# Performance work log

Hardware: AMD Instinct MI355X
Metric: run time of the kernel (lower is better)

Reference implementation:

```python
import jax, jax.numpy as jnp
import numpy as np

B, T, D = 8, 1024, 512
H = 8
F_OUT = D // H          # 64 per head
ALPHA = 0.2             # LeakyReLU slope in GAT
MASK_RATE = 0.3
GAMMA = 0.0625          # DistanceAdj gamma
BIAS = 0.2              # DistanceAdj bias
LN_EPS = 1e-5
NEG_INF = -9e15
L2_EPS = 1e-12          # F.normalize eps


def setup_inputs() -> dict:
    key = jax.random.key(0)
    ks = jax.random.split(key, 8)
    return {
        "x": jax.random.normal(ks[0], (B, T, D), jnp.float32),
        "W": jax.random.normal(ks[1], (H, D, F_OUT), jnp.float32) * 0.05,
        "a_src": jax.random.normal(ks[2], (H, F_OUT), jnp.float32) * 0.05,
        "a_dst": jax.random.normal(ks[3], (H, F_OUT), jnp.float32) * 0.05,
        "W2": jax.random.normal(ks[4], (D, D), jnp.float32) * 0.02,
        "b2": jnp.zeros((D,), jnp.float32),
        "ln_g": jnp.ones((D,), jnp.float32),
        "ln_b": jnp.zeros((D,), jnp.float32),
    }


def _distance_adj(batch, t):
    # DistanceAdj: Gaussian kernel over temporal index distance, shared across batch
    idx = jnp.arange(t, dtype=jnp.float32)
    d2 = (idx[:, None] - idx[None, :]) ** 2
    adj = jnp.exp(-GAMMA * d2 - BIAS)                      # [T, T]
    return jnp.broadcast_to(adj[None], (batch, t, t))      # [B, T, T]


def reference(x, W, a_src, a_dst, W2, b2, ln_g, ln_b):
    b, t, d = x.shape
    adj = _distance_adj(b, t)

    # top-k magnitude node selection -> row/col union mask (index_fill loop)
    k = int(MASK_RATE * t)
    mags = jnp.linalg.norm(x, axis=2)                      # [B, T]
    _, topk = jax.lax.top_k(mags, k)                       # [B, k]
    sel = jnp.zeros((b, t), bool).at[jnp.arange(b)[:, None], topk].set(True)
    mask = sel[:, :, None] | sel[:, None, :]               # rows OR cols filled
    adj = jnp.where(mask, adj, 0.0)

    # GAT multi-head attention (dense masked form, dropout=0 at eval)
    Wh = jnp.einsum("btd,hdf->bhtf", x, W)                 # [B,H,T,F']
    e_src = jnp.einsum("bhtf,hf->bht", Wh, a_src)
    e_dst = jnp.einsum("bhtf,hf->bht", Wh, a_dst)
    e = jax.nn.leaky_relu(e_src[..., :, None] + e_dst[..., None, :], ALPHA)
    e = jnp.where(adj[:, None] > 0, e, NEG_INF)            # masked logits
    attn = jax.nn.softmax(e, axis=-1)                      # [B,H,T,T]
    hp = jnp.einsum("bhts,bhsf->bhtf", attn, Wh)
    hp = jax.nn.elu(hp)                                    # concat=True -> elu per head
    tmp = hp.transpose(0, 2, 1, 3).reshape(b, t, d)        # concat heads -> [B,T,512]

    # signed-sqrt + F.normalize (default dim=1 -> over T axis)
    tmp = jnp.sqrt(jax.nn.relu(tmp)) - jnp.sqrt(jax.nn.relu(-tmp))
    nrm = jnp.linalg.norm(tmp, axis=1, keepdims=True)      # [B,1,D]
    tmp = tmp / jnp.maximum(nrm, L2_EPS)

    # residual linear + LayerNorm + permute
    y = x + tmp @ W2 + b2
    mu = jnp.mean(y, axis=-1, keepdims=True)
    var = jnp.mean((y - mu) ** 2, axis=-1, keepdims=True)
    y = (y - mu) / jnp.sqrt(var + LN_EPS) * ln_g + ln_b
    return y.transpose(0, 2, 1)                            # [B, D, T]
```

## Files before the change

kernel.cpp:

```cpp
#include <hip/hip_runtime.h>
#include <hip/hip_bf16.h>

typedef unsigned short u16;
typedef short bf16x8 __attribute__((ext_vector_type(8)));
typedef float f32x4 __attribute__((ext_vector_type(4)));
typedef int   i32x4 __attribute__((ext_vector_type(4)));

#define NB 8
#define NT 1024
#define ND 512
#define KSEL 307
#define PSTR 152
#define TSTR 136

__device__ __forceinline__ float bf2f(u16 u){
  union { unsigned int i; float f; } c; c.i = ((unsigned int)u) << 16; return c.f;
}
__device__ __forceinline__ u16 f2bf(float f){
  __hip_bfloat16 h = __float2bfloat16(f);
  u16 u; __builtin_memcpy(&u, &h, 2); return u;
}

__global__ void k_select(const float* __restrict__ mags, int* __restrict__ sel){
  __shared__ float sm[NT];
  int b = blockIdx.x;
  int tid = threadIdx.x;
  for (int i = tid; i < NT; i += 256) sm[i] = mags[b * NT + i];
  __syncthreads();
  int tl = tid >> 2, tq = tid & 3;
  int t = blockIdx.y * 64 + tl;
  float m = sm[t];
  int cnt = 0;
  int s0 = tq * 256;
  for (int s = s0; s < s0 + 256; s++){
    float v = sm[s];
    cnt += (v > m) || (v == m && s < t);
  }
  cnt += __shfl_xor(cnt, 1, 64);
  cnt += __shfl_xor(cnt, 2, 64);
  if (tq == 0) sel[b * NT + t] = (cnt < KSEL) ? 1 : 0;
}

__launch_bounds__(256, 3)
__global__ void k_gemm_wh(const float* __restrict__ x, const float* __restrict__ Wf,
                          const float* __restrict__ W2f,
                          const float* __restrict__ a_src, const float* __restrict__ a_dst,
                          u16* __restrict__ WhT, float* __restrict__ es, float* __restrict__ ed,
                          float* __restrict__ mags, float* __restrict__ cn,
                          u16* __restrict__ W2T){
  __shared__ u16 smem[8704];
  u16* As = smem;
  u16* Bs = smem + 5120;
  int m0 = blockIdx.x * 128;
  int h  = blockIdx.y;
  int tid = threadIdx.x;
  if (h == 0 && tid < 64) cn[blockIdx.x * 64 + tid] = 0.f;
  if (h == 2){
    float* tile = (float*)smem;
    int kt0 = (blockIdx.x >> 3) * 64, n00 = (blockIdx.x & 7) * 64;
    int r = tid >> 6, cl = tid & 63;
#pragma unroll
    for (int p = 0; p < 16; p++)
      tile[(r + p*4)*65 + cl] = W2f[(size_t)(kt0 + r + p*4) * 512 + n00 + cl];
    __syncthreads();
#pragma unroll
    for (int p = 0; p < 16; p++){
      int orow = r + p*4;
      W2T[(size_t)(n00 + orow) * 512 + kt0 + cl] = f2bf(tile[cl*65 + orow]);
    }
    __syncthreads();
  }
  int wv = tid >> 6, lane = tid & 63;
  int quad = lane >> 4, lr = lane & 15;
  f32x4 acc[2][4] = {};
  float sq[2] = {0.f, 0.f};
  int ar = (tid * 8) >> 5, ac = (tid * 8) & 31;
  const float* xa0 = &x[(size_t)(m0 + ar) * 512 + ac];
  const float* xa1 = xa0 + (size_t)64 * 512;
  int kk = (tid * 8) >> 6, f0 = (tid * 8) & 63;
  const float* wb = &Wf[((size_t)h << 15) + (size_t)kk * 64 + f0];
  int bbase = f0 * 40 + (((kk >> 3) ^ ((f0 >> 3) & 3)) * 8) + (kk & 7);
  f32x4 pa0 = *(const f32x4*)xa0, pa1 = *(const f32x4*)(xa0 + 4);
  f32x4 pa2 = *(const f32x4*)xa1, pa3 = *(const f32x4*)(xa1 + 4);
  f32x4 pb0 = *(const f32x4*)wb,  pb1 = *(const f32x4*)(wb + 4);
  for (int kt = 0; kt < 512; kt += 32){
    __syncthreads();
    {
      u16 pk[8];
      if (h == 0){
#pragma unroll
        for (int q = 0; q < 4; q++) sq[0] += pa0[q]*pa0[q] + pa1[q]*pa1[q];
#pragma unroll
        for (int q = 0; q < 4; q++) sq[1] += pa2[q]*pa2[q] + pa3[q]*pa3[q];
      }
#pragma unroll
      for (int q = 0; q < 4; q++){ pk[q] = f2bf(pa0[q]); pk[4+q] = f2bf(pa1[q]); }
      *(bf16x8*)&As[ar*40 + ac] = *(const bf16x8*)pk;
#pragma unroll
      for (int q = 0; q < 4; q++){ pk[q] = f2bf(pa2[q]); pk[4+q] = f2bf(pa3[q]); }
      *(bf16x8*)&As[(ar + 64)*40 + ac] = *(const bf16x8*)pk;
#pragma unroll
      for (int q = 0; q < 4; q++) Bs[bbase + q*40]       = f2bf(pb0[q]);
#pragma unroll
      for (int q = 0; q < 4; q++) Bs[bbase + (q+4)*40]   = f2bf(pb1[q]);
    }
    __syncthreads();
    if (kt < 480){
      pa0 = *(const f32x4*)(xa0 + kt + 32); pa1 = *(const f32x4*)(xa0 + kt + 36);
      pa2 = *(const f32x4*)(xa1 + kt + 32); pa3 = *(const f32x4*)(xa1 + kt + 36);
      pb0 = *(const f32x4*)(wb + (size_t)(kt + 32) * 64);
      pb1 = *(const f32x4*)(wb + (size_t)(kt + 32) * 64 + 4);
    }
    bf16x8 af[2], bfr[4];
#pragma unroll
    for (int i = 0; i < 2; i++) af[i] = *(const bf16x8*)&As[(wv*32 + i*16 + lr)*40 + quad*8];
#pragma unroll
    for (int i = 0; i < 4; i++){
      int f = i*16 + lr;
      bfr[i] = *(const bf16x8*)&Bs[f*40 + ((quad ^ ((f >> 3) & 3)) * 8)];
    }
#pragma unroll
    for (int mi = 0; mi < 2; mi++)
#pragma unroll
      for (int ni = 0; ni < 4; ni++)
        acc[mi][ni] = __builtin_amdgcn_mfma_f32_16x16x32_bf16(af[mi], bfr[ni], acc[mi][ni], 0, 0, 0);
  }
  if (h == 0){
#pragma unroll
    for (int i = 0; i < 2; i++){
      float s = sq[i];
      s += __shfl_xor(s, 1, 64);
      s += __shfl_xor(s, 2, 64);
      if ((tid & 3) == 0) mags[m0 + i*64 + (tid >> 2)] = sqrtf(s);
    }
  }
  float asv[4], adv[4];
#pragma unroll
  for (int ni = 0; ni < 4; ni++){
    asv[ni] = a_src[h*64 + ni*16 + lr];
    adv[ni] = a_dst[h*64 + ni*16 + lr];
  }
#pragma unroll
  for (int mi = 0; mi < 2; mi++)
#pragma unroll
    for (int r = 0; r < 4; r++){
      float pes = 0.f, ped = 0.f;
#pragma unroll
      for (int ni = 0; ni < 4; ni++){
        pes += acc[mi][ni][r] * asv[ni];
        ped += acc[mi][ni][r] * adv[ni];
      }
#pragma unroll
      for (int mofs = 1; mofs < 16; mofs <<= 1){
        pes += __shfl_xor(pes, mofs, 64);
        ped += __shfl_xor(ped, mofs, 64);
      }
      if (lr == 0){
        int rowg = m0 + wv*32 + mi*16 + quad*4 + r;
        int bb_ = rowg >> 10, tt = rowg & 1023;
        es[(bb_ * 8 + h) * NT + tt] = pes;
        ed[(bb_ * 8 + h) * NT + tt] = ped;
      }
    }
  __syncthreads();
  u16* Tr = smem;
#pragma unroll
  for (int mi = 0; mi < 2; mi++)
#pragma unroll
    for (int ni = 0; ni < 4; ni++){
      int fl = ni*16 + lr;
      int tl = wv*32 + mi*16 + quad*4;
#pragma unroll
      for (int r = 0; r < 4; r++) Tr[fl*TSTR + tl + r] = f2bf(acc[mi][ni][r]);
    }
  __syncthreads();
  int f = tid >> 2, seg = tid & 3;
  int b_ = m0 >> 10;
  u16* dst = &WhT[(b_ * 512 + h * 64 + f) * NT + (m0 & 1023) + seg*32];
  const u16* srcp = &Tr[f*TSTR + seg*32];
#pragma unroll
  for (int k8 = 0; k8 < 4; k8++)
    *(bf16x8*)(dst + k8*8) = *(const bf16x8*)(srcp + k8*8);
}

__launch_bounds__(256)
__global__ void k_attn(const u16* __restrict__ WhT, const float* __restrict__ es,
                       const float* __restrict__ ed, const int* __restrict__ sel,
                       u16* __restrict__ t2b, float* __restrict__ cn){
  __shared__ u16 P[64 * PSTR];
  __shared__ float edw[144];
  __shared__ int   selw[144];
  __shared__ float esw[64];
  __shared__ float swv[64];
  int bh = blockIdx.x;
  int b = bh >> 3;
  int t0 = blockIdx.y * 64;
  int tid = threadIdx.x;
  int wv = tid >> 6, lane = tid & 63;
  int quad = lane >> 4, lr = lane & 15;
  int s_base = t0 - 40;
  for (int i = tid; i < 144; i += 256){
    int s = s_base + i;
    bool ok = (s >= 0 && s < NT);
    edw[i]  = ok ? ed[bh * NT + s] : 0.f;
    selw[i] = ok ? sel[b * NT + s] : 0;
  }
  if (tid < 64) esw[tid] = es[bh * NT + t0 + tid];
  {
    i32x4 z = {};
    for (int i = lane; i < 304; i += 64){
      int r16 = i / 19, c16 = i - r16 * 19;
      *(i32x4*)&P[(16*wv + r16) * PSTR + c16 * 8] = z;
    }
  }
  __syncthreads();
  {
    int tl = 16*wv + (lane >> 2);
    int q = lane & 3;
    float e_t = esw[tl];
    int sel_t = selw[tl + 40];
    float part = 0.f;
    for (int j = q; j <= 80; j += 4){
      int sw = tl + j;
      int s = s_base + sw;
      float w = 0.f;
      if (s >= 0 && s < NT && (sel_t | selw[sw])){
        float v = e_t + edw[sw];
        v = v > 0.f ? v : 0.2f * v;
        v = fminf(v, 60.f);
        w = bf2f(f2bf(__expf(v)));
      }
      part += w;
      if (w != 0.f) P[tl * PSTR + sw] = f2bf(w);
    }
    part += __shfl_xor(part, 1, 64);
    part += __shfl_xor(part, 2, 64);
    if (q == 0) swv[tl] = part;
  }
  __syncthreads();
  f32x4 acc[4] = {};
  const u16* vbase = WhT + (bh * 64) * NT;
#pragma unroll
  for (int ks = 0; ks < 96; ks += 32){
    bf16x8 afr = *(const bf16x8*)&P[(16*wv + lr) * PSTR + 16*wv + ks + quad*8];
    int tb = s_base + 16*wv + ks + quad*8;
    bool ok = (tb >= 0) && (tb < NT);
    bf16x8 zf = {};
#pragma unroll
    for (int jn = 0; jn < 4; jn++){
      bf16x8 bfr = ok ? *(const bf16x8*)&vbase[(16*jn + lr) * NT + tb] : zf;
      acc[jn] = __builtin_amdgcn_mfma_f32_16x16x32_bf16(afr, bfr, acc[jn], 0, 0, 0);
    }
  }
#pragma unroll
  for (int jn = 0; jn < 4; jn++){
    float ssum = 0.f;
#pragma unroll
    for (int r = 0; r < 4; r++){
      int t_loc = 16*wv + quad*4 + r;
      float sw_ = swv[t_loc];
      float hp = acc[jn][r] / (sw_ > 0.f ? sw_ : 1.f);
      hp = hp > 0.f ? hp : (__expf(hp) - 1.f);
      float o = hp >= 0.f ? sqrtf(hp) : -sqrtf(-hp);
      ssum += o * o;
      t2b[(b * NT + t0 + t_loc) * ND + (bh & 7) * 64 + 16*jn + lr] = f2bf(o);
    }
    ssum += __shfl_xor(ssum, 16, 64);
    ssum += __shfl_xor(ssum, 32, 64);
    if (quad == 0) atomicAdd(&cn[b * ND + (bh & 7) * 64 + 16*jn + lr], ssum);
  }
}

__launch_bounds__(512)
__global__ void k_gemm2ln(const u16* __restrict__ A, const u16* __restrict__ W2T,
                          const float* __restrict__ xres, const float* __restrict__ b2,
                          const float* __restrict__ cn, const float* __restrict__ g,
                          const float* __restrict__ bb, float* __restrict__ out){
  __shared__ __align__(16) char smraw[69888];
  u16*   As  = (u16*)smraw;
  u16*   Bs  = (u16*)(smraw + 2560);
  float* scl = (float*)(smraw + 43520);
  float* T     = (float*)smraw;
  float* wpart = (float*)(smraw + 67584);
  float* mus   = (float*)(smraw + 69632);
  float* rss   = (float*)(smraw + 69760);
  int tid = threadIdx.x;
  int m0 = blockIdx.x * 32;
  int b  = m0 >> 10, t0 = m0 & 1023;
  int w = tid >> 6, lane = tid & 63;
  int quad = lane >> 4, lr = lane & 15;
  {
    float nv = sqrtf(cn[(b << 9) + tid]);
    scl[tid] = 1.f / fmaxf(nv, 1e-12f);
  }
  int ar = tid >> 2, ac = (tid & 3) * 8;
  const u16* ap = &A[(size_t)(m0 + ar) * 512 + ac];
  int nb_ = tid >> 2, c = (tid & 3) * 8;
  bf16x8 ra = {}, rb[4];
  if (tid < 128) ra = __builtin_nontemporal_load((const bf16x8*)ap);
#pragma unroll
  for (int rep = 0; rep < 4; rep++)
    rb[rep] = *(const bf16x8*)&W2T[(size_t)(nb_ + rep*128) * 512 + c];
  f32x4 acc[2][4] = {};
  for (int kt = 0; kt < 512; kt += 32){
    __syncthreads();
    if (tid < 128){
      u16 pk[8];
#pragma unroll
      for (int q = 0; q < 8; q++)
        pk[q] = f2bf(bf2f((u16)ra[q]) * scl[kt + ac + q]);
      *(bf16x8*)&As[ar*40 + ac] = *(const bf16x8*)pk;
    }
#pragma unroll
    for (int rep = 0; rep < 4; rep++)
      *(bf16x8*)&Bs[(nb_ + rep*128)*40 + c] = rb[rep];
    __syncthreads();
    if (kt < 480){
      if (tid < 128) ra = __builtin_nontemporal_load((const bf16x8*)(ap + kt + 32));
#pragma unroll
      for (int rep = 0; rep < 4; rep++)
        rb[rep] = *(const bf16x8*)&W2T[(size_t)(nb_ + rep*128) * 512 + kt + 32 + c];
    }
    bf16x8 af[2], bfr[4];
#pragma unroll
    for (int mi = 0; mi < 2; mi++) af[mi] = *(const bf16x8*)&As[(mi*16 + lr)*40 + quad*8];
#pragma unroll
    for (int i = 0; i < 4; i++)
      bfr[i] = *(const bf16x8*)&Bs[(w*64 + i*16 + lr)*40 + quad*8];
#pragma unroll
    for (int mi = 0; mi < 2; mi++)
#pragma unroll
      for (int ni = 0; ni < 4; ni++)
        acc[mi][ni] = __builtin_amdgcn_mfma_f32_16x16x32_bf16(af[mi], bfr[ni], acc[mi][ni], 0, 0, 0);
  }
  float b2v[4];
#pragma unroll
  for (int ni = 0; ni < 4; ni++) b2v[ni] = b2[w*64 + ni*16 + lr];
  float yv[2][4][4];
#pragma unroll
  for (int mi = 0; mi < 2; mi++)
#pragma unroll
    for (int r = 0; r < 4; r++){
      int rl = mi*16 + quad*4 + r;
      float rs = 0.f, rq = 0.f;
#pragma unroll
      for (int ni = 0; ni < 4; ni++){
        int col = w*64 + ni*16 + lr;
        float v = acc[mi][ni][r]
                + __builtin_nontemporal_load(&xres[(size_t)(m0 + rl) * 512 + col])
                + b2v[ni];
        yv[mi][ni][r] = v;
        rs += v; rq += v * v;
      }
#pragma unroll
      for (int m2 = 1; m2 < 16; m2 <<= 1){
        rs += __shfl_xor(rs, m2, 64);
        rq += __shfl_xor(rq, m2, 64);
      }
      if (lr == 0){
        wpart[w*32 + rl]       = rs;
        wpart[256 + w*32 + rl] = rq;
      }
    }
  __syncthreads();
  if (tid < 32){
    float s = 0.f, q = 0.f;
#pragma unroll
    for (int wv2 = 0; wv2 < 8; wv2++){
      s += wpart[wv2*32 + tid];
      q += wpart[256 + wv2*32 + tid];
    }
    float mu = s * (1.f/512.f);
    float var = q * (1.f/512.f) - mu * mu;
    mus[tid] = mu;
    rss[tid] = 1.f / sqrtf(var + 1e-5f);
  }
  __syncthreads();
  float gv[4], bv[4];
#pragma unroll
  for (int ni = 0; ni < 4; ni++){
    gv[ni] = g[w*64 + ni*16 + lr];
    bv[ni] = bb[w*64 + ni*16 + lr];
  }
#pragma unroll
  for (int mi = 0; mi < 2; mi++)
#pragma unroll
    for (int r = 0; r < 4; r++){
      int rl = mi*16 + quad*4 + r;
      float mu = mus[rl], rstd = rss[rl];
#pragma unroll
      for (int ni = 0; ni < 4; ni++){
        int col = w*64 + ni*16 + lr;
        T[col*33 + rl] = (yv[mi][ni][r] - mu) * rstd * gv[ni] + bv[ni];
      }
    }
  __syncthreads();
  int j = tid & 31, dq = tid >> 5;
#pragma unroll
  for (int kk2 = 0; kk2 < 32; kk2++){
    int d = dq + kk2 * 16;
    __builtin_nontemporal_store(T[d*33 + j],
        &out[((size_t)(b * 512 + d)) * 1024 + t0 + j]);
  }
}

extern "C" void kernel_launch(void* const* d_in, const int* in_sizes, int n_in,
                              void* d_out, int out_size, void* d_ws, size_t ws_size,
                              hipStream_t stream) {
  (void)in_sizes; (void)n_in; (void)out_size; (void)ws_size;
  const float* x     = (const float*)d_in[0];
  const float* W     = (const float*)d_in[1];
  const float* a_src = (const float*)d_in[2];
  const float* a_dst = (const float*)d_in[3];
  const float* W2    = (const float*)d_in[4];
  const float* b2    = (const float*)d_in[5];
  const float* ln_g  = (const float*)d_in[6];
  const float* ln_b  = (const float*)d_in[7];
  char* ws = (char*)d_ws;
  int*   sel   = (int*)  (ws + 256);
  float* mags  = (float*)(ws + 33024);
  float* es    = (float*)(ws + 1124608);
  float* ed    = (float*)(ws + 1386752);
  float* cn    = (float*)(ws + 1648896);
  u16*   WhT   = (u16*)  (ws + 2097152);
  u16*   t2b   = (u16*)  (ws + 18874368);
  u16*   W2T   = (u16*)  (ws + 36175872);
  float* out   = (float*)d_out;

  k_gemm_wh  <<<dim3(64, 8), 256, 0, stream>>>(x, W, W2, a_src, a_dst, WhT, es, ed, mags, cn, W2T);
  k_select   <<<dim3(NB, 16), 256, 0, stream>>>(mags, sel);
  k_attn     <<<dim3(64, 16), 256, 0, stream>>>(WhT, es, ed, sel, t2b, cn);
  k_gemm2ln  <<<dim3(256), 512, 0, stream>>>(t2b, W2T, x, b2, cn, ln_g, ln_b, out);
}
```

Baseline: 144.0 us.

## Split K of output GEMM across two thread groups in 1024-thread blocks

The W2 projection+LayerNorm kernel now launches 1024 threads per block, and two 512-thread groups each handle half of the K dimension with separate LDS tiles. The second group writes its partial accumulators to shared memory, where the first group sums them before the residual, LayerNorm and transposed store. The aim is to halve the serial K loop per block and raise wave count with only 256 blocks in the grid. In exchange it uses more shared memory per block, adds an LDS reduction and extra barriers, and leaves half the threads idle during the epilogue.

Result: no change. 144.0 us (+0.0%).

```diff
diff --git a/kernel.cpp b/kernel.cpp
--- a/kernel.cpp
+++ b/kernel.cpp
@@ -271,55 +271,63 @@
   }
 }
 
-__launch_bounds__(512)
+__launch_bounds__(1024, 4)
 __global__ void k_gemm2ln(const u16* __restrict__ A, const u16* __restrict__ W2T,
                           const float* __restrict__ xres, const float* __restrict__ b2,
                           const float* __restrict__ cn, const float* __restrict__ g,
                           const float* __restrict__ bb, float* __restrict__ out){
-  __shared__ __align__(16) char smraw[69888];
-  u16*   As  = (u16*)smraw;
-  u16*   Bs  = (u16*)(smraw + 2560);
-  float* scl = (float*)(smraw + 43520);
-  float* T     = (float*)smraw;
-  float* wpart = (float*)(smraw + 67584);
-  float* mus   = (float*)(smraw + 69632);
-  float* rss   = (float*)(smraw + 69760);
+  __shared__ __align__(16) char smraw[91392];
+  u16* As0 = (u16*)smraw;
+  u16* As1 = (u16*)(smraw + 2560);
+  u16* Bs0 = (u16*)(smraw + 5120);
+  u16* Bs1 = (u16*)(smraw + 46080);
+  float* scl   = (float*)(smraw + 87040);
+  float* wpart = (float*)(smraw + 89088);
+  float* mus   = (float*)(smraw + 91136);
+  float* rss   = (float*)(smraw + 91264);
+  float* accbuf = (float*)(smraw + 5120);
+  float* T      = (float*)smraw;
   int tid = threadIdx.x;
+  int gid = tid >> 9;
+  int l   = tid & 511;
   int m0 = blockIdx.x * 32;
   int b  = m0 >> 10, t0 = m0 & 1023;
-  int w = tid >> 6, lane = tid & 63;
-  int quad = lane >> 4, lr = lane & 15;
-  {
+  int w = l >> 6;
+  int lane = tid & 63, quad = lane >> 4, lr = lane & 15;
+  u16* As = gid ? As1 : As0;
+  u16* Bs = gid ? Bs1 : Bs0;
+  int kb = gid << 8;
+  if (tid < 512){
     float nv = sqrtf(cn[(b << 9) + tid]);
     scl[tid] = 1.f / fmaxf(nv, 1e-12f);
   }
-  int ar = tid >> 2, ac = (tid & 3) * 8;
-  const u16* ap = &A[(size_t)(m0 + ar) * 512 + ac];
-  int nb_ = tid >> 2, c = (tid & 3) * 8;
+  int ar = l >> 2, ac = (l & 3) * 8;
+  const u16* ap = &A[(size_t)(m0 + ar) * 512 + kb + ac];
+  int nb_ = l >> 2, c = (l & 3) * 8;
   bf16x8 ra = {}, rb[4];
-  if (tid < 128) ra = __builtin_nontemporal_load((const bf16x8*)ap);
+  if (l < 128) ra = *(const bf16x8*)ap;
 #pragma unroll
   for (int rep = 0; rep < 4; rep++)
-    rb[rep] = *(const bf16x8*)&W2T[(size_t)(nb_ + rep*128) * 512 + c];
+    rb[rep] = *(const bf16x8*)&W2T[(size_t)(nb_ + rep*128) * 512 + kb + c];
   f32x4 acc[2][4] = {};
-  for (int kt = 0; kt < 512; kt += 32){
-    __syncthreads();
-    if (tid < 128){
+  for (int kt = 0; kt < 256; kt += 32){
+    __syncthreads();
+    if (l < 128){
       u16 pk[8];
 #pragma unroll
       for (int q = 0; q < 8; q++)
-        pk[q] = f2bf(bf2f((u16)ra[q]) * scl[kt + ac + q]);
+        pk[q] = f2bf(bf2f((u16)ra[q]) * scl[kb + kt + ac + q]);
       *(bf16x8*)&As[ar*40 + ac] = *(const bf16x8*)pk;
     }
 #pragma unroll
     for (int rep = 0; rep < 4; rep++)
       *(bf16x8*)&Bs[(nb_ + rep*128)*40 + c] = rb[rep];
     __syncthreads();
-    if (kt < 480){
-      if (tid < 128) ra = __builtin_nontemporal_load((const bf16x8*)(ap + kt + 32));
+    if (kt < 224){
+      if (l < 128) ra = *(const bf16x8*)(ap + kt + 32);
 #pragma unroll
       for (int rep = 0; rep < 4; rep++)
-        rb[rep] = *(const bf16x8*)&W2T[(size_t)(nb_ + rep*128) * 512 + kt + 32 + c];
+        rb[rep] = *(const bf16x8*)&W2T[(size_t)(nb_ + rep*128) * 512 + kb + kt + 32 + c];
     }
     bf16x8 af[2], bfr[4];
 #pragma unroll
@@ -333,35 +341,49 @@
       for (int ni = 0; ni < 4; ni++)
         acc[mi][ni] = __builtin_amdgcn_mfma_f32_16x16x32_bf16(af[mi], bfr[ni], acc[mi][ni], 0, 0, 0);
   }
-  float b2v[4];
-#pragma unroll
-  for (int ni = 0; ni < 4; ni++) b2v[ni] = b2[w*64 + ni*16 + lr];
+  __syncthreads();
+  if (gid == 1){
+    float* dst = &accbuf[l * 33];
+#pragma unroll
+    for (int mi = 0; mi < 2; mi++)
+#pragma unroll
+      for (int ni = 0; ni < 4; ni++)
+#pragma unroll
+        for (int r = 0; r < 4; r++)
+          dst[mi*16 + ni*4 + r] = acc[mi][ni][r];
+  }
+  __syncthreads();
   float yv[2][4][4];
-#pragma unroll
-  for (int mi = 0; mi < 2; mi++)
-#pragma unroll
-    for (int r = 0; r < 4; r++){
-      int rl = mi*16 + quad*4 + r;
-      float rs = 0.f, rq = 0.f;
-#pragma unroll
-      for (int ni = 0; ni < 4; ni++){
-        int col = w*64 + ni*16 + lr;
-        float v = acc[mi][ni][r]
-                + __builtin_nontemporal_load(&xres[(size_t)(m0 + rl) * 512 + col])
-                + b2v[ni];
-        yv[mi][ni][r] = v;
-        rs += v; rq += v * v;
-      }
-#pragma unroll
-      for (int m2 = 1; m2 < 16; m2 <<= 1){
-        rs += __shfl_xor(rs, m2, 64);
-        rq += __shfl_xor(rq, m2, 64);
-      }
-      if (lr == 0){
-        wpart[w*32 + rl]       = rs;
-        wpart[256 + w*32 + rl] = rq;
-      }
-    }
+  if (gid == 0){
+    const float* src = &accbuf[l * 33];
+    float b2v[4];
+#pragma unroll
+    for (int ni = 0; ni < 4; ni++) b2v[ni] = b2[w*64 + ni*16 + lr];
+#pragma unroll
+    for (int mi = 0; mi < 2; mi++)
+#pragma unroll
+      for (int r = 0; r < 4; r++){
+        int rl = mi*16 + quad*4 + r;
+        float rs = 0.f, rq = 0.f;
+#pragma unroll
+        for (int ni = 0; ni < 4; ni++){
+          int col = w*64 + ni*16 + lr;
+          float v = acc[mi][ni][r] + src[mi*16 + ni*4 + r]
+                  + xres[(size_t)(m0 + rl) * 512 + col] + b2v[ni];
+          yv[mi][ni][r] = v;
+          rs += v; rq += v * v;
+        }
+#pragma unroll
+        for (int m2 = 1; m2 < 16; m2 <<= 1){
+          rs += __shfl_xor(rs, m2, 64);
+          rq += __shfl_xor(rq, m2, 64);
+        }
+        if (lr == 0){
+          wpart[w*32 + rl]       = rs;
+          wpart[256 + w*32 + rl] = rq;
+        }
+      }
+  }
   __syncthreads();
   if (tid < 32){
     float s = 0.f, q = 0.f;
@@ -376,29 +398,31 @@
     rss[tid] = 1.f / sqrtf(var + 1e-5f);
   }
   __syncthreads();
-  float gv[4], bv[4];
-#pragma unroll
-  for (int ni = 0; ni < 4; ni++){
-    gv[ni] = g[w*64 + ni*16 + lr];
-    bv[ni] = bb[w*64 + ni*16 + lr];
-  }
-#pragma unroll
-  for (int mi = 0; mi < 2; mi++)
-#pragma unroll
-    for (int r = 0; r < 4; r++){
-      int rl = mi*16 + quad*4 + r;
-      float mu = mus[rl], rstd = rss[rl];
-#pragma unroll
-      for (int ni = 0; ni < 4; ni++){
-        int col = w*64 + ni*16 + lr;
-        T[col*33 + rl] = (yv[mi][ni][r] - mu) * rstd * gv[ni] + bv[ni];
-      }
-    }
+  if (gid == 0){
+    float gv[4], bv[4];
+#pragma unroll
+    for (int ni = 0; ni < 4; ni++){
+      gv[ni] = g[w*64 + ni*16 + lr];
+      bv[ni] = bb[w*64 + ni*16 + lr];
+    }
+#pragma unroll
+    for (int mi = 0; mi < 2; mi++)
+#pragma unroll
+      for (int r = 0; r < 4; r++){
+        int rl = mi*16 + quad*4 + r;
+        float mu = mus[rl], rstd = rss[rl];
+#pragma unroll
+        for (int ni = 0; ni < 4; ni++){
+          int col = w*64 + ni*16 + lr;
+          T[col*33 + rl] = (yv[mi][ni][r] - mu) * rstd * gv[ni] + bv[ni];
+        }
+      }
+  }
   __syncthreads();
   int j = tid & 31, dq = tid >> 5;
 #pragma unroll
-  for (int kk2 = 0; kk2 < 32; kk2++){
-    int d = dq + kk2 * 16;
+  for (int kk2 = 0; kk2 < 16; kk2++){
+    int d = dq + kk2 * 32;
     __builtin_nontemporal_store(T[d*33 + j],
         &out[((size_t)(b * 512 + d)) * 1024 + t0 + j]);
   }
@@ -430,5 +454,5 @@
   k_gemm_wh  <<<dim3(64, 8), 256, 0, stream>>>(x, W, W2, a_src, a_dst, WhT, es, ed, mags, cn, W2T);
   k_select   <<<dim3(NB, 16), 256, 0, stream>>>(mags, sel);
   k_attn     <<<dim3(64, 16), 256, 0, stream>>>(WhT, es, ed, sel, t2b, cn);
-  k_gemm2ln  <<<dim3(256), 512, 0, stream>>>(t2b, W2T, x, b2, cn, ln_g, ln_b, out);
-}
+  k_gemm2ln  <<<dim3(256), 1024, 0, stream>>>(t2b, W2T, x, b2, cn, ln_g, ln_b, out);
+}
```
